# Kernel optimization log

Hardware: AMD Instinct MI355X
Metric: run time of the kernel (lower is better)

The kernel has to match this reference:

```python
import jax, jax.numpy as jnp
import numpy as np


def setup_inputs() -> dict:
    key = jax.random.key(0)
    k1, k2, k3, k4, k5 = jax.random.split(key, 5)
    B, n_vis, n_hid, n_target = 16384, 2048, 512, 2
    return {
        "input_data": jax.random.normal(k1, (B, n_vis), dtype=jnp.float32),
        "W": jax.random.normal(k2, (n_hid, n_vis), dtype=jnp.float32),
        "U": jax.random.normal(k3, (n_hid, n_target), dtype=jnp.float32),
        "h_bias": jax.random.normal(k4, (1, n_hid), dtype=jnp.float32),
        "y_bias": jax.random.normal(k5, (1, n_target), dtype=jnp.float32),
    }


def reference(input_data, W, U, h_bias, y_bias):
    # precomputed_factor: [B, n_hid]
    pf = input_data @ W.T + h_bias
    # logits[b, c] = y_bias[c] + sum_j softplus(pf[b, j] + U[j, c])
    # broadcast to [B, n_hid, n_target], reduce over hidden dim
    sp = jax.nn.softplus(pf[:, :, None] + U[None, :, :])  # [B, n_hid, n_target]
    logits = y_bias + sp.sum(axis=1)  # [B, n_target]
    # the double class loop computes 1 / sum_d exp(logits_d - logits_c) == softmax
    return jax.nn.softmax(logits, axis=1)
```

## Files before the change

kernel.cpp:

```cpp
#include <hip/hip_runtime.h>
#include <hip/hip_bf16.h>
#include <hip/hip_fp16.h>
#include <stdint.h>

typedef __attribute__((ext_vector_type(8))) _Float16 f16x8;
typedef __attribute__((ext_vector_type(4))) float f32x4;
typedef __attribute__((ext_vector_type(4))) int i32x4;

#define GLD_LDS16(g, l) __builtin_amdgcn_global_load_lds( \
    (const __attribute__((address_space(1))) uint32_t*)(g), \
    (__attribute__((address_space(3))) uint32_t*)(l), 16, 0, 0)

__global__ __launch_bounds__(256) void k_cvt_w(const float* __restrict__ W,
                                               _Float16* __restrict__ Wh) {
  int i = (blockIdx.x * 256 + threadIdx.x) * 8;
  float4 a = *(const float4*)(W + i);
  float4 b = *(const float4*)(W + i + 4);
  union { _Float16 h[8]; i32x4 v; } u;
  u.h[0] = (_Float16)a.x; u.h[1] = (_Float16)a.y;
  u.h[2] = (_Float16)a.z; u.h[3] = (_Float16)a.w;
  u.h[4] = (_Float16)b.x; u.h[5] = (_Float16)b.y;
  u.h[6] = (_Float16)b.z; u.h[7] = (_Float16)b.w;
  *(i32x4*)(Wh + i) = u.v;
}

__device__ inline float softplus_f(float x) {
  float e = __expf(-fabsf(x));
  return fmaxf(x, 0.f) + __logf(1.f + e);
}

__global__ __launch_bounds__(512, 2) void k_main(
    const float* __restrict__ X,
    const _Float16* __restrict__ Wh,
    const float* __restrict__ U,
    const float* __restrict__ hb,
    float* __restrict__ Dp) {
  __shared__ __align__(16) _Float16 As[2][128 * 64];
  __shared__ __align__(16) _Float16 Bs[3][256 * 64];
  __shared__ float sD[128];

  const int t = threadIdx.x;
  const int lane = t & 63;
  const int wid = t >> 6;
  const int wm = wid >> 2;
  const int wn = wid & 3;
  const int bx = blockIdx.x;
  const int rt = (bx >> 4) * 8 + (bx & 7);
  const int nhalf = (bx >> 3) & 1;
  const int bm0 = rt * 128;
  const int bn0 = nhalf * 256;
  const int lrow = lane & 15, lq = lane >> 4;

  if (t < 128) sD[t] = 0.f;
  __syncthreads();

  f32x4 acc[4][4];
#pragma unroll
  for (int m = 0; m < 4; ++m)
#pragma unroll
    for (int n = 0; n < 4; ++n) acc[m][n] = (f32x4){0.f, 0.f, 0.f, 0.f};

  const int arow = t >> 2, ach = t & 3;
  const float* xsrc = X + (size_t)(bm0 + arow) * 2048 + ach * 16;
  const int c0 = ach * 2;
  const int aw0 = arow * 128 + (((c0) ^ (arow & 7)) << 4);
  const int aw1 = arow * 128 + (((c0 + 1) ^ (arow & 7)) << 4);

  const int l8 = lane >> 3, s8 = lane & 7;
  const _Float16* bsrc =
      Wh + (size_t)(bn0 + wid * 32 + l8) * 2048 + (s8 ^ l8) * 8;
  char* const bd0 = (char*)&Bs[0][0] + wid * 4096;
  char* const bd1 = (char*)&Bs[1][0] + wid * 4096;
  char* const bd2 = (char*)&Bs[2][0] + wid * 4096;

  f32x4 arA[4], arB[4];

#define CVT_WRITE_A(ARC, Q) do {                                           \
    f16x8 hv0, hv1;                                                        \
    _Pragma("unroll") for (int j = 0; j < 4; ++j) {                        \
      hv0[j] = (_Float16)ARC[0][j]; hv0[j + 4] = (_Float16)ARC[1][j];      \
      hv1[j] = (_Float16)ARC[2][j]; hv1[j + 4] = (_Float16)ARC[3][j];      \
    }                                                                      \
    *(f16x8*)((char*)&As[Q][0] + aw0) = hv0;                               \
    *(f16x8*)((char*)&As[Q][0] + aw1) = hv1;                               \
  } while (0)

#define FRAGS(P, BR, KS, FA, FB) do {                                      \
    _Pragma("unroll") for (int mf = 0; mf < 4; ++mf) {                     \
      int row = wm * 64 + mf * 16 + lrow;                                  \
      int off = row * 128 + ((((KS)*4 + lq) ^ (row & 7)) << 4);            \
      FA[mf] = *(const f16x8*)((const char*)&As[P][0] + off);              \
    }                                                                      \
    _Pragma("unroll") for (int nf = 0; nf < 4; ++nf) {                     \
      int row = wn * 64 + nf * 16 + lrow;                                  \
      int off = row * 128 + ((((KS)*4 + lq) ^ (row & 7)) << 4);            \
      FB[nf] = *(const f16x8*)((const char*)&Bs[BR][0] + off);             \
    }                                                                      \
  } while (0)

#define MFMA16(FA, FB) do {                                                \
    __builtin_amdgcn_s_setprio(1);                                         \
    _Pragma("unroll") for (int mf = 0; mf < 4; ++mf)                       \
      _Pragma("unroll") for (int nf = 0; nf < 4; ++nf)                     \
        acc[mf][nf] = __builtin_amdgcn_mfma_f32_16x16x32_f16(              \
            FA[mf], FB[nf], acc[mf][nf], 0, 0, 0);                         \
    __builtin_amdgcn_s_setprio(0);                                         \
  } while (0)

#define STEP(KT, P, Q, ARL, ARC, BR, BWD) do {                             \
    const int kb_ = ((KT) + 2 > 31) ? 31 : (KT) + 2;                       \
    {                  \
      f16x8 fa[4], fb[4];                                                  \
      FRAGS(P, BR, 0, fa, fb);                                             \
      _Pragma("unroll") for (int i = 0; i < 4; ++i)                        \
        GLD_LDS16(bsrc + (size_t)i * 16384 + (size_t)kb_ * 64,             \
                  (BWD) + i * 1024);                                       \
      __builtin_amdgcn_s_barrier();                                        \
      asm volatile("s_waitcnt lgkmcnt(0)" ::: "memory");                   \
      __builtin_amdgcn_sched_barrier(0);                                   \
      MFMA16(fa, fb);                                                      \
      __builtin_amdgcn_s_barrier();                                        \
    }                                                                      \
    {       \
      f16x8 fa[4], fb[4];                                                  \
      FRAGS(P, BR, 1, fa, fb);                                             \
      _Pragma("unroll") for (int c = 0; c < 4; ++c)                        \
        ARL[c] = *(const f32x4*)(xsrc + (size_t)kb_ * 64 + c * 4);         \
      CVT_WRITE_A(ARC, Q);                                                 \
      asm volatile("s_waitcnt vmcnt(8) lgkmcnt(0)" ::: "memory");          \
      __builtin_amdgcn_sched_barrier(0);                                   \
      __builtin_amdgcn_s_barrier();                                        \
      MFMA16(fa, fb);                                                      \
      __builtin_amdgcn_s_barrier();                                        \
    }                                                                      \
  } while (0)

#pragma unroll
  for (int i = 0; i < 4; ++i)
    GLD_LDS16(bsrc + (size_t)i * 16384, bd0 + i * 1024);
#pragma unroll
  for (int i = 0; i < 4; ++i)
    GLD_LDS16(bsrc + (size_t)i * 16384 + 64, bd1 + i * 1024);
#pragma unroll
  for (int c = 0; c < 4; ++c) arA[c] = *(const f32x4*)(xsrc + c * 4);
#pragma unroll
  for (int c = 0; c < 4; ++c) arB[c] = *(const f32x4*)(xsrc + 64 + c * 4);
  CVT_WRITE_A(arA, 0);
  asm volatile("s_waitcnt vmcnt(4) lgkmcnt(0)" ::: "memory");
  __builtin_amdgcn_s_barrier();

  for (int kt = 0; kt < 30; kt += 6) {
    STEP(kt + 0, 0, 1, arA, arB, 0, bd2);
    STEP(kt + 1, 1, 0, arB, arA, 1, bd0);
    STEP(kt + 2, 0, 1, arA, arB, 2, bd1);
    STEP(kt + 3, 1, 0, arB, arA, 0, bd2);
    STEP(kt + 4, 0, 1, arA, arB, 1, bd0);
    STEP(kt + 5, 1, 0, arB, arA, 2, bd1);
  }
  STEP(30, 0, 1, arA, arB, 0, bd2);
  STEP(31, 1, 0, arB, arA, 1, bd0);
#undef STEP
#undef MFMA16
#undef FRAGS
#undef CVT_WRITE_A

  float dpart[16];
#pragma unroll
  for (int i = 0; i < 16; ++i) dpart[i] = 0.f;
#pragma unroll
  for (int nf = 0; nf < 4; ++nf) {
    int h = bn0 + wn * 64 + nf * 16 + lrow;
    float hbv = hb[h];
    float u0 = U[2 * h], u1 = U[2 * h + 1];
#pragma unroll
    for (int mf = 0; mf < 4; ++mf)
#pragma unroll
      for (int r = 0; r < 4; ++r) {
        float pf = acc[mf][nf][r] + hbv;
        dpart[mf * 4 + r] += softplus_f(pf + u0) - softplus_f(pf + u1);
      }
  }
#pragma unroll
  for (int i = 0; i < 16; ++i) {
    float v = dpart[i];
    v += __shfl_xor(v, 1);
    v += __shfl_xor(v, 2);
    v += __shfl_xor(v, 4);
    v += __shfl_xor(v, 8);
    dpart[i] = v;
  }
  if (lrow == 0) {
#pragma unroll
    for (int mf = 0; mf < 4; ++mf)
#pragma unroll
      for (int r = 0; r < 4; ++r)
        atomicAdd(&sD[wm * 64 + mf * 16 + lq * 4 + r], dpart[mf * 4 + r]);
  }
  __syncthreads();
  if (t < 128) Dp[nhalf * 16384 + bm0 + t] = sD[t];
}

__global__ __launch_bounds__(256) void k_final(const float* __restrict__ Dp,
                                               const float* __restrict__ yb,
                                               float* __restrict__ out) {
  int i = blockIdx.x * 256 + threadIdx.x;
  float D = Dp[i] + Dp[16384 + i] + yb[0] - yb[1];
  float e = __expf(-D);
  float o0 = 1.f / (1.f + e);
  float o1 = e * o0;
  *(float2*)(out + (size_t)i * 2) = make_float2(o0, o1);
}

extern "C" void kernel_launch(void* const* d_in, const int* in_sizes, int n_in,
                              void* d_out, int out_size, void* d_ws,
                              size_t ws_size, hipStream_t stream) {
  const float* X = (const float*)d_in[0];
  const float* W = (const float*)d_in[1];
  const float* U = (const float*)d_in[2];
  const float* hb = (const float*)d_in[3];
  const float* yb = (const float*)d_in[4];
  float* out = (float*)d_out;
  _Float16* Wh = (_Float16*)d_ws;
  float* Dp = (float*)((char*)d_ws + 2 * 1024 * 1024);

  hipLaunchKernelGGL(k_cvt_w, dim3(512), dim3(256), 0, stream, W, Wh);
  hipLaunchKernelGGL(k_main, dim3(256), dim3(512), 0, stream, X, Wh, U, hb, Dp);
  hipLaunchKernelGGL(k_final, dim3(64), dim3(256), 0, stream, Dp, yb, out);
}
```

Measured before the change: 64.29 us.

## Triple-buffer A tile and software-pipeline LDS fragment loads across k-steps

Grows the A shared-memory buffer from two to three stages. Each k-step now loads the next step's k-slice-0 fragments while the current MFMAs run, and cuts the barriers per step from four to one. The goal is to hide LDS read latency and barrier stalls behind MFMA work. The cost is more LDS, which may lower occupancy at two blocks per CU, and more live fragment registers. The per-step ordering of lgkm waits is now implicit, which risks races if the compiler reorders instructions.

```diff
diff --git a/kernel.cpp b/kernel.cpp
--- a/kernel.cpp
+++ b/kernel.cpp
@@ -35,7 +35,7 @@
     const float* __restrict__ U,
     const float* __restrict__ hb,
     float* __restrict__ Dp) {
-  __shared__ __align__(16) _Float16 As[2][128 * 64];
+  __shared__ __align__(16) _Float16 As[3][128 * 64];
   __shared__ __align__(16) _Float16 Bs[3][256 * 64];
   __shared__ float sD[128];
 
@@ -52,7 +52,6 @@
   const int lrow = lane & 15, lq = lane >> 4;
 
   if (t < 128) sD[t] = 0.f;
-  __syncthreads();
 
   f32x4 acc[4][4];
 #pragma unroll
@@ -74,6 +73,7 @@
   char* const bd2 = (char*)&Bs[2][0] + wid * 4096;
 
   f32x4 arA[4], arB[4];
+  f16x8 fa0[4], fb0[4], fa1[4], fb1[4];
 
 #define CVT_WRITE_A(ARC, Q) do {                                           \
     f16x8 hv0, hv1;                                                        \
@@ -85,16 +85,19 @@
     *(f16x8*)((char*)&As[Q][0] + aw1) = hv1;                               \
   } while (0)
 
-#define FRAGS(P, BR, KS, FA, FB) do {                                      \
+#define FRAGS_A(P, KS, FA) do {                                            \
     _Pragma("unroll") for (int mf = 0; mf < 4; ++mf) {                     \
       int row = wm * 64 + mf * 16 + lrow;                                  \
       int off = row * 128 + ((((KS)*4 + lq) ^ (row & 7)) << 4);            \
       FA[mf] = *(const f16x8*)((const char*)&As[P][0] + off);              \
     }                                                                      \
+  } while (0)
+
+#define FRAGS_B(P, KS, FB) do {                                            \
     _Pragma("unroll") for (int nf = 0; nf < 4; ++nf) {                     \
       int row = wn * 64 + nf * 16 + lrow;                                  \
       int off = row * 128 + ((((KS)*4 + lq) ^ (row & 7)) << 4);            \
-      FB[nf] = *(const f16x8*)((const char*)&Bs[BR][0] + off);             \
+      FB[nf] = *(const f16x8*)((const char*)&Bs[P][0] + off);              \
     }                                                                      \
   } while (0)
 
@@ -107,32 +110,23 @@
     __builtin_amdgcn_s_setprio(0);                                         \
   } while (0)
 
-#define STEP(KT, P, Q, ARL, ARC, BR, BWD) do {                             \
+#define STEP(KT, ARL, ARC, P, Pn, Pw, BDW) do {                            \
     const int kb_ = ((KT) + 2 > 31) ? 31 : (KT) + 2;                       \
-    {                  \
-      f16x8 fa[4], fb[4];                                                  \
-      FRAGS(P, BR, 0, fa, fb);                                             \
-      _Pragma("unroll") for (int i = 0; i < 4; ++i)                        \
-        GLD_LDS16(bsrc + (size_t)i * 16384 + (size_t)kb_ * 64,             \
-                  (BWD) + i * 1024);                                       \
-      __builtin_amdgcn_s_barrier();                                        \
-      asm volatile("s_waitcnt lgkmcnt(0)" ::: "memory");                   \
-      __builtin_amdgcn_sched_barrier(0);                                   \
-      MFMA16(fa, fb);                                                      \
-      __builtin_amdgcn_s_barrier();                                        \
-    }                                                                      \
-    {       \
-      f16x8 fa[4], fb[4];                                                  \
-      FRAGS(P, BR, 1, fa, fb);                                             \
-      _Pragma("unroll") for (int c = 0; c < 4; ++c)                        \
-        ARL[c] = *(const f32x4*)(xsrc + (size_t)kb_ * 64 + c * 4);         \
-      CVT_WRITE_A(ARC, Q);                                                 \
-      asm volatile("s_waitcnt vmcnt(8) lgkmcnt(0)" ::: "memory");          \
-      __builtin_amdgcn_sched_barrier(0);                                   \
-      __builtin_amdgcn_s_barrier();                                        \
-      MFMA16(fa, fb);                                                      \
-      __builtin_amdgcn_s_barrier();                                        \
-    }                                                                      \
+    const int ka_ = ((KT) + 3 > 31) ? 31 : (KT) + 3;                       \
+    _Pragma("unroll") for (int i = 0; i < 4; ++i)         \
+      GLD_LDS16(bsrc + (size_t)i * 16384 + (size_t)kb_ * 64,               \
+                (BDW) + i * 1024);                                         \
+    _Pragma("unroll") for (int c = 0; c < 4; ++c)     \
+      ARL[c] = *(const f32x4*)(xsrc + (size_t)ka_ * 64 + c * 4);           \
+    FRAGS_A(P, 1, fa1);                                 \
+    FRAGS_B(P, 1, fb1);                                                    \
+    MFMA16(fa0, fb0);                                  \
+    CVT_WRITE_A(ARC, Pw);                              \
+    FRAGS_A(Pn, 0, fa0);                               \
+    MFMA16(fa1, fb1);                                                      \
+    asm volatile("s_waitcnt vmcnt(8)" ::: "memory");    \
+    __builtin_amdgcn_s_barrier();                                          \
+    FRAGS_B(Pn, 0, fb0);                               \
   } while (0)
 
 #pragma unroll
@@ -143,25 +137,31 @@
     GLD_LDS16(bsrc + (size_t)i * 16384 + 64, bd1 + i * 1024);
 #pragma unroll
   for (int c = 0; c < 4; ++c) arA[c] = *(const f32x4*)(xsrc + c * 4);
-#pragma unroll
-  for (int c = 0; c < 4; ++c) arB[c] = *(const f32x4*)(xsrc + 64 + c * 4);
   CVT_WRITE_A(arA, 0);
-  asm volatile("s_waitcnt vmcnt(4) lgkmcnt(0)" ::: "memory");
+#pragma unroll
+  for (int c = 0; c < 4; ++c) arA[c] = *(const f32x4*)(xsrc + 64 + c * 4);
+  CVT_WRITE_A(arA, 1);
+#pragma unroll
+  for (int c = 0; c < 4; ++c) arA[c] = *(const f32x4*)(xsrc + 128 + c * 4);
+  asm volatile("s_waitcnt vmcnt(0) lgkmcnt(0)" ::: "memory");
   __builtin_amdgcn_s_barrier();
+  FRAGS_A(0, 0, fa0);
+  FRAGS_B(0, 0, fb0);
 
   for (int kt = 0; kt < 30; kt += 6) {
-    STEP(kt + 0, 0, 1, arA, arB, 0, bd2);
-    STEP(kt + 1, 1, 0, arB, arA, 1, bd0);
-    STEP(kt + 2, 0, 1, arA, arB, 2, bd1);
-    STEP(kt + 3, 1, 0, arB, arA, 0, bd2);
-    STEP(kt + 4, 0, 1, arA, arB, 1, bd0);
-    STEP(kt + 5, 1, 0, arB, arA, 2, bd1);
-  }
-  STEP(30, 0, 1, arA, arB, 0, bd2);
-  STEP(31, 1, 0, arB, arA, 1, bd0);
+    STEP(kt + 0, arB, arA, 0, 1, 2, bd2);
+    STEP(kt + 1, arA, arB, 1, 2, 0, bd0);
+    STEP(kt + 2, arB, arA, 2, 0, 1, bd1);
+    STEP(kt + 3, arA, arB, 0, 1, 2, bd2);
+    STEP(kt + 4, arB, arA, 1, 2, 0, bd0);
+    STEP(kt + 5, arA, arB, 2, 0, 1, bd1);
+  }
+  STEP(30, arB, arA, 0, 1, 2, bd2);
+  STEP(31, arA, arB, 1, 2, 0, bd0);
 #undef STEP
 #undef MFMA16
-#undef FRAGS
+#undef FRAGS_A
+#undef FRAGS_B
 #undef CVT_WRITE_A
 
   float dpart[16];
```

Result: slower. 65.88 us (+2.5%).

## Shrink main GEMM tile to 128x128 with 256 threads and 4-way N split

Applied to the files above, without the earlier changes.

Changes the main kernel from 128x256 tiles with 512 threads to 128x128 tiles with 256 threads, launching 512 blocks and splitting the hidden dimension four ways. Partial sums are combined in the final kernel. The B buffer drops from triple to double buffering, and the A prefetch is split across both half-steps, so LDS use falls and more blocks can be resident. The cost is that each X row tile is now read and converted four times instead of twice.

```diff
diff --git a/kernel.cpp b/kernel.cpp
--- a/kernel.cpp
+++ b/kernel.cpp
@@ -29,30 +29,29 @@
   return fmaxf(x, 0.f) + __logf(1.f + e);
 }
 
-__global__ __launch_bounds__(512, 2) void k_main(
+__global__ __launch_bounds__(256, 2) void k_main(
     const float* __restrict__ X,
     const _Float16* __restrict__ Wh,
     const float* __restrict__ U,
     const float* __restrict__ hb,
     float* __restrict__ Dp) {
   __shared__ __align__(16) _Float16 As[2][128 * 64];
-  __shared__ __align__(16) _Float16 Bs[3][256 * 64];
+  __shared__ __align__(16) _Float16 Bs[2][128 * 64];
   __shared__ float sD[128];
 
   const int t = threadIdx.x;
   const int lane = t & 63;
   const int wid = t >> 6;
-  const int wm = wid >> 2;
-  const int wn = wid & 3;
+  const int wm = wid >> 1;
+  const int wn = wid & 1;
   const int bx = blockIdx.x;
-  const int rt = (bx >> 4) * 8 + (bx & 7);
-  const int nhalf = (bx >> 3) & 1;
+  const int rt = (bx >> 5) * 8 + (bx & 7);
+  const int nq = (bx >> 3) & 3;
   const int bm0 = rt * 128;
-  const int bn0 = nhalf * 256;
+  const int bn0 = nq * 128;
   const int lrow = lane & 15, lq = lane >> 4;
 
   if (t < 128) sD[t] = 0.f;
-  __syncthreads();
 
   f32x4 acc[4][4];
 #pragma unroll
@@ -60,32 +59,43 @@
 #pragma unroll
     for (int n = 0; n < 4; ++n) acc[m][n] = (f32x4){0.f, 0.f, 0.f, 0.f};
 
-  const int arow = t >> 2, ach = t & 3;
-  const float* xsrc = X + (size_t)(bm0 + arow) * 2048 + ach * 16;
-  const int c0 = ach * 2;
-  const int aw0 = arow * 128 + (((c0) ^ (arow & 7)) << 4);
-  const int aw1 = arow * 128 + (((c0 + 1) ^ (arow & 7)) << 4);
+  const int arow = t >> 1;
+  const float* xsrc = X + (size_t)(bm0 + arow) * 2048 + (t & 1) * 32;
+  const int c0 = (t & 1) * 4;
+  int awc[4];
+#pragma unroll
+  for (int j = 0; j < 4; ++j)
+    awc[j] = arow * 128 + (((c0 + j) ^ (arow & 7)) << 4);
 
   const int l8 = lane >> 3, s8 = lane & 7;
   const _Float16* bsrc =
       Wh + (size_t)(bn0 + wid * 32 + l8) * 2048 + (s8 ^ l8) * 8;
   char* const bd0 = (char*)&Bs[0][0] + wid * 4096;
   char* const bd1 = (char*)&Bs[1][0] + wid * 4096;
-  char* const bd2 = (char*)&Bs[2][0] + wid * 4096;
-
-  f32x4 arA[4], arB[4];
-
-#define CVT_WRITE_A(ARC, Q) do {                                           \
+
+  f32x4 ah0A[4], ah1A[4], ah0B[4], ah1B[4];
+
+#define CVT_H0(ARR, Q) do {                                                \
     f16x8 hv0, hv1;                                                        \
     _Pragma("unroll") for (int j = 0; j < 4; ++j) {                        \
-      hv0[j] = (_Float16)ARC[0][j]; hv0[j + 4] = (_Float16)ARC[1][j];      \
-      hv1[j] = (_Float16)ARC[2][j]; hv1[j + 4] = (_Float16)ARC[3][j];      \
-    }                                                                      \
-    *(f16x8*)((char*)&As[Q][0] + aw0) = hv0;                               \
-    *(f16x8*)((char*)&As[Q][0] + aw1) = hv1;                               \
-  } while (0)
-
-#define FRAGS(P, BR, KS, FA, FB) do {                                      \
+      hv0[j] = (_Float16)ARR[0][j]; hv0[j + 4] = (_Float16)ARR[1][j];      \
+      hv1[j] = (_Float16)ARR[2][j]; hv1[j + 4] = (_Float16)ARR[3][j];      \
+    }                                                                      \
+    *(f16x8*)((char*)&As[Q][0] + awc[0]) = hv0;                            \
+    *(f16x8*)((char*)&As[Q][0] + awc[1]) = hv1;                            \
+  } while (0)
+
+#define CVT_H1(ARR, Q) do {                                                \
+    f16x8 hv0, hv1;                                                        \
+    _Pragma("unroll") for (int j = 0; j < 4; ++j) {                        \
+      hv0[j] = (_Float16)ARR[0][j]; hv0[j + 4] = (_Float16)ARR[1][j];      \
+      hv1[j] = (_Float16)ARR[2][j]; hv1[j + 4] = (_Float16)ARR[3][j];      \
+    }                                                                      \
+    *(f16x8*)((char*)&As[Q][0] + awc[2]) = hv0;                            \
+    *(f16x8*)((char*)&As[Q][0] + awc[3]) = hv1;                            \
+  } while (0)
+
+#define FRAGS(P, KS, FA, FB) do {                                          \
     _Pragma("unroll") for (int mf = 0; mf < 4; ++mf) {                     \
       int row = wm * 64 + mf * 16 + lrow;                                  \
       int off = row * 128 + ((((KS)*4 + lq) ^ (row & 7)) << 4);            \
@@ -94,7 +104,7 @@
     _Pragma("unroll") for (int nf = 0; nf < 4; ++nf) {                     \
       int row = wn * 64 + nf * 16 + lrow;                                  \
       int off = row * 128 + ((((KS)*4 + lq) ^ (row & 7)) << 4);            \
-      FB[nf] = *(const f16x8*)((const char*)&Bs[BR][0] + off);             \
+      FB[nf] = *(const f16x8*)((const char*)&Bs[P][0] + off);              \
     }                                                                      \
   } while (0)
 
@@ -107,26 +117,30 @@
     __builtin_amdgcn_s_setprio(0);                                         \
   } while (0)
 
-#define STEP(KT, P, Q, ARL, ARC, BR, BWD) do {                             \
-    const int kb_ = ((KT) + 2 > 31) ? 31 : (KT) + 2;                       \
-    {                  \
+#define STEP(KT, P, Q, H0L, H1L, H0C, H1C, BDQ) do {                       \
+    const int kb_ = ((KT) + 1 > 31) ? 31 : (KT) + 1;                       \
+    const int ka_ = ((KT) + 2 > 31) ? 31 : (KT) + 2;                       \
+    {                                                         \
       f16x8 fa[4], fb[4];                                                  \
-      FRAGS(P, BR, 0, fa, fb);                                             \
-      _Pragma("unroll") for (int i = 0; i < 4; ++i)                        \
-        GLD_LDS16(bsrc + (size_t)i * 16384 + (size_t)kb_ * 64,             \
-                  (BWD) + i * 1024);                                       \
+      FRAGS(P, 0, fa, fb);                                                 \
+      _Pragma("unroll") for (int i = 0; i < 4; ++i)           \
+        GLD_LDS16(bsrc + (size_t)i * 8 * 2048 + (size_t)kb_ * 64,          \
+                  (BDQ) + i * 1024);                                       \
+      _Pragma("unroll") for (int c = 0; c < 4; ++c)        \
+        H0L[c] = *(const f32x4*)(xsrc + (size_t)ka_ * 64 + c * 4);         \
+      CVT_H0(H0C, Q);                                      \
       __builtin_amdgcn_s_barrier();                                        \
       asm volatile("s_waitcnt lgkmcnt(0)" ::: "memory");                   \
       __builtin_amdgcn_sched_barrier(0);                                   \
       MFMA16(fa, fb);                                                      \
       __builtin_amdgcn_s_barrier();                                        \
     }                                                                      \
-    {       \
+    {                                                         \
       f16x8 fa[4], fb[4];                                                  \
-      FRAGS(P, BR, 1, fa, fb);                                             \
-      _Pragma("unroll") for (int c = 0; c < 4; ++c)                        \
-        ARL[c] = *(const f32x4*)(xsrc + (size_t)kb_ * 64 + c * 4);         \
-      CVT_WRITE_A(ARC, Q);                                                 \
+      FRAGS(P, 1, fa, fb);                                                 \
+      _Pragma("unroll") for (int c = 0; c < 4; ++c)        \
+        H1L[c] = *(const f32x4*)(xsrc + (size_t)ka_ * 64 + 16 + c * 4);    \
+      CVT_H1(H1C, Q);                                      \
       asm volatile("s_waitcnt vmcnt(8) lgkmcnt(0)" ::: "memory");          \
       __builtin_amdgcn_sched_barrier(0);                                   \
       __builtin_amdgcn_s_barrier();                                        \
@@ -137,32 +151,29 @@
 
 #pragma unroll
   for (int i = 0; i < 4; ++i)
-    GLD_LDS16(bsrc + (size_t)i * 16384, bd0 + i * 1024);
-#pragma unroll
-  for (int i = 0; i < 4; ++i)
-    GLD_LDS16(bsrc + (size_t)i * 16384 + 64, bd1 + i * 1024);
-#pragma unroll
-  for (int c = 0; c < 4; ++c) arA[c] = *(const f32x4*)(xsrc + c * 4);
-#pragma unroll
-  for (int c = 0; c < 4; ++c) arB[c] = *(const f32x4*)(xsrc + 64 + c * 4);
-  CVT_WRITE_A(arA, 0);
-  asm volatile("s_waitcnt vmcnt(4) lgkmcnt(0)" ::: "memory");
+    GLD_LDS16(bsrc + (size_t)i * 8 * 2048, bd0 + i * 1024);
+#pragma unroll
+  for (int c = 0; c < 4; ++c) ah0A[c] = *(const f32x4*)(xsrc + c * 4);
+#pragma unroll
+  for (int c = 0; c < 4; ++c) ah1A[c] = *(const f32x4*)(xsrc + 16 + c * 4);
+#pragma unroll
+  for (int c = 0; c < 4; ++c) ah0B[c] = *(const f32x4*)(xsrc + 64 + c * 4);
+#pragma unroll
+  for (int c = 0; c < 4; ++c) ah1B[c] = *(const f32x4*)(xsrc + 80 + c * 4);
+  CVT_H0(ah0A, 0);
+  CVT_H1(ah1A, 0);
+  asm volatile("s_waitcnt lgkmcnt(0)" ::: "memory");
   __builtin_amdgcn_s_barrier();
 
-  for (int kt = 0; kt < 30; kt += 6) {
-    STEP(kt + 0, 0, 1, arA, arB, 0, bd2);
-    STEP(kt + 1, 1, 0, arB, arA, 1, bd0);
-    STEP(kt + 2, 0, 1, arA, arB, 2, bd1);
-    STEP(kt + 3, 1, 0, arB, arA, 0, bd2);
-    STEP(kt + 4, 0, 1, arA, arB, 1, bd0);
-    STEP(kt + 5, 1, 0, arB, arA, 2, bd1);
-  }
-  STEP(30, 0, 1, arA, arB, 0, bd2);
-  STEP(31, 1, 0, arB, arA, 1, bd0);
+  for (int kt = 0; kt < 32; kt += 2) {
+    STEP(kt, 0, 1, ah0A, ah1A, ah0B, ah1B, bd1);
+    STEP(kt + 1, 1, 0, ah0B, ah1B, ah0A, ah1A, bd0);
+  }
 #undef STEP
 #undef MFMA16
 #undef FRAGS
-#undef CVT_WRITE_A
+#undef CVT_H0
+#undef CVT_H1
 
   float dpart[16];
 #pragma unroll
@@ -197,14 +208,15 @@
         atomicAdd(&sD[wm * 64 + mf * 16 + lq * 4 + r], dpart[mf * 4 + r]);
   }
   __syncthreads();
-  if (t < 128) Dp[nhalf * 16384 + bm0 + t] = sD[t];
+  if (t < 128) Dp[nq * 16384 + bm0 + t] = sD[t];
 }
 
 __global__ __launch_bounds__(256) void k_final(const float* __restrict__ Dp,
                                                const float* __restrict__ yb,
                                                float* __restrict__ out) {
   int i = blockIdx.x * 256 + threadIdx.x;
-  float D = Dp[i] + Dp[16384 + i] + yb[0] - yb[1];
+  float D = Dp[i] + Dp[16384 + i] + Dp[2 * 16384 + i] + Dp[3 * 16384 + i] +
+            yb[0] - yb[1];
   float e = __expf(-D);
   float o0 = 1.f / (1.f + e);
   float o1 = e * o0;
@@ -224,6 +236,7 @@
   float* Dp = (float*)((char*)d_ws + 2 * 1024 * 1024);
 
   hipLaunchKernelGGL(k_cvt_w, dim3(512), dim3(256), 0, stream, W, Wh);
-  hipLaunchKernelGGL(k_main, dim3(256), dim3(512), 0, stream, X, Wh, U, hb, Dp);
+  hipLaunchKernelGGL(k_main, dim3(512), dim3(256), 0, stream, X, Wh, U, hb,
+                     Dp);
   hipLaunchKernelGGL(k_final, dim3(64), dim3(256), 0, stream, Dp, yb, out);
 }
```

New measurement: 97.06 us. +51.0%, slower.
